# Performance work log

Hardware: AMD Instinct MI355X
Metric: run time of the kernel (lower is better)

## Reference

```python
import jax, jax.numpy as jnp
import numpy as np

EMBED = 64
HEADS = 4
HEAD_DIM = EMBED // HEADS
N, T = 1024, 36


def setup_inputs() -> dict:
    key = jax.random.key(0)
    ks = jax.random.split(key, 8)
    scale = 1.0 / np.sqrt(HEAD_DIM)
    return {
        "values": jax.random.normal(ks[0], (N, T, EMBED), dtype=jnp.float32),
        "keys": jax.random.normal(ks[1], (N, T, EMBED), dtype=jnp.float32),
        "query": jax.random.normal(ks[2], (N, T, EMBED), dtype=jnp.float32),
        "Wv": jax.random.normal(ks[3], (HEAD_DIM, HEAD_DIM), dtype=jnp.float32) * scale,
        "Wk": jax.random.normal(ks[4], (HEAD_DIM, HEAD_DIM), dtype=jnp.float32) * scale,
        "Wq": jax.random.normal(ks[5], (HEAD_DIM, HEAD_DIM), dtype=jnp.float32) * scale,
        "Wo": jax.random.normal(ks[6], (EMBED, EMBED), dtype=jnp.float32) * (1.0 / np.sqrt(EMBED)),
        "bo": jax.random.normal(ks[7], (EMBED,), dtype=jnp.float32) * 0.01,
    }


def reference(values, keys, query, Wv, Wk, Wq, Wo, bo):
    n, t, c = query.shape
    h, d = HEADS, HEAD_DIM
    v = values.reshape(n, t, h, d)
    k = keys.reshape(n, t, h, d)
    q = query.reshape(n, t, h, d)
    # nn.Linear(head_dim, head_dim, bias=False): x @ W.T
    v = jnp.einsum('nthd,ed->nthe', v, Wv)
    k = jnp.einsum('nthd,ed->nthe', k, Wk)
    q = jnp.einsum('nthd,ed->nthe', q, Wq)
    # attention over the node dim: energy [N_q, N_k, T, H]
    energy = jnp.einsum('qthd,kthd->qkth', q, k)
    attention = jax.nn.softmax(energy / jnp.sqrt(jnp.float32(c)), axis=1)
    out = jnp.einsum('qkth,kthd->qthd', attention, v).reshape(n, t, h * d)
    return out @ Wo.T + bo
```

## Files before the change

kernel.cpp:

```cpp
#include <hip/hip_runtime.h>
#include <math.h>

#define N_NODES 1024
#define T_STEPS 36
#define KTILE   128
#define KSTR2   24
#define VTSTR   136
#define WOS     72
#define OBS2    72

typedef __bf16  bf16x8 __attribute__((ext_vector_type(8)));
typedef float   f32x4  __attribute__((ext_vector_type(4)));

#define MFMA_BF16 __builtin_amdgcn_mfma_f32_16x16x32_bf16

__device__ __forceinline__ unsigned short bf16_rne(float f) {
    unsigned int u = __float_as_uint(f);
    u += 0x7FFFu + ((u >> 16) & 1u);
    return (unsigned short)(u >> 16);
}
__device__ __forceinline__ float bf16_tof(unsigned short h) {
    return __uint_as_float(((unsigned int)h) << 16);
}
__device__ __forceinline__ unsigned int bf16_bias(float f) {
    unsigned int u = __float_as_uint(f);
    return u + 0x7FFFu + ((u >> 16) & 1u);
}

__global__ __launch_bounds__(128) void proj4_kernel(
    const float* __restrict__ vin, const float* __restrict__ kin, const float* __restrict__ qin,
    const float* __restrict__ Wv, const float* __restrict__ Wk, const float* __restrict__ Wq,
    unsigned short* __restrict__ qhi, unsigned short* __restrict__ qlo,
    unsigned short* __restrict__ khi, unsigned short* __restrict__ klo,
    unsigned short* __restrict__ vthi, unsigned short* __restrict__ vtlo)
{
    __shared__ float sWv[256], sWk[256], sWq[256];
    const int tid = threadIdx.x;
    sWv[tid] = Wv[tid]; sWv[tid+128] = Wv[tid+128];
    sWk[tid] = Wk[tid]; sWk[tid+128] = Wk[tid+128];
    sWq[tid] = Wq[tid]; sWq[tid+128] = Wq[tid+128];
    __syncthreads();

    const int t = blockIdx.y;
    const int n = blockIdx.x * 128 + tid;
    const size_t ib = ((size_t)n * T_STEPS + t) * 64;
    const float QSCALE = 0.18033688011112042f;

    float x[64], y[4][16];

    #pragma unroll
    for (int i = 0; i < 16; ++i) { float4 f = *(const float4*)(qin + ib + 4*i);
        x[4*i]=f.x; x[4*i+1]=f.y; x[4*i+2]=f.z; x[4*i+3]=f.w; }
    #pragma unroll
    for (int e = 0; e < 16; ++e) {
        float4 w0 = *(const float4*)&sWq[e*16+0],  w1 = *(const float4*)&sWq[e*16+4];
        float4 w2 = *(const float4*)&sWq[e*16+8],  w3 = *(const float4*)&sWq[e*16+12];
        #pragma unroll
        for (int hd = 0; hd < 4; ++hd) {
            const float* xr = &x[hd*16];
            float a = xr[0]*w0.x;
            a = fmaf(xr[1],w0.y,a);  a = fmaf(xr[2],w0.z,a);  a = fmaf(xr[3],w0.w,a);
            a = fmaf(xr[4],w1.x,a);  a = fmaf(xr[5],w1.y,a);  a = fmaf(xr[6],w1.z,a);  a = fmaf(xr[7],w1.w,a);
            a = fmaf(xr[8],w2.x,a);  a = fmaf(xr[9],w2.y,a);  a = fmaf(xr[10],w2.z,a); a = fmaf(xr[11],w2.w,a);
            a = fmaf(xr[12],w3.x,a); a = fmaf(xr[13],w3.y,a); a = fmaf(xr[14],w3.z,a); a = fmaf(xr[15],w3.w,a);
            y[hd][e] = a * QSCALE;
        }
    }
    #pragma unroll
    for (int hd = 0; hd < 4; ++hd) {
        union { unsigned short u[16]; uint4 v[2]; } hb, lb;
        #pragma unroll
        for (int e = 0; e < 16; ++e) { unsigned short hh = bf16_rne(y[hd][e]);
            hb.u[e] = hh; lb.u[e] = bf16_rne(y[hd][e] - bf16_tof(hh)); }
        uint4* dh = (uint4*)(qhi + ((size_t)(t*4+hd)*N_NODES + n)*16);
        uint4* dl = (uint4*)(qlo + ((size_t)(t*4+hd)*N_NODES + n)*16);
        dh[0]=hb.v[0]; dh[1]=hb.v[1]; dl[0]=lb.v[0]; dl[1]=lb.v[1];
    }

    #pragma unroll
    for (int i = 0; i < 16; ++i) { float4 f = *(const float4*)(kin + ib + 4*i);
        x[4*i]=f.x; x[4*i+1]=f.y; x[4*i+2]=f.z; x[4*i+3]=f.w; }
    #pragma unroll
    for (int e = 0; e < 16; ++e) {
        float4 w0 = *(const float4*)&sWk[e*16+0],  w1 = *(const float4*)&sWk[e*16+4];
        float4 w2 = *(const float4*)&sWk[e*16+8],  w3 = *(const float4*)&sWk[e*16+12];
        #pragma unroll
        for (int hd = 0; hd < 4; ++hd) {
            const float* xr = &x[hd*16];
            float a = xr[0]*w0.x;
            a = fmaf(xr[1],w0.y,a);  a = fmaf(xr[2],w0.z,a);  a = fmaf(xr[3],w0.w,a);
            a = fmaf(xr[4],w1.x,a);  a = fmaf(xr[5],w1.y,a);  a = fmaf(xr[6],w1.z,a);  a = fmaf(xr[7],w1.w,a);
            a = fmaf(xr[8],w2.x,a);  a = fmaf(xr[9],w2.y,a);  a = fmaf(xr[10],w2.z,a); a = fmaf(xr[11],w2.w,a);
            a = fmaf(xr[12],w3.x,a); a = fmaf(xr[13],w3.y,a); a = fmaf(xr[14],w3.z,a); a = fmaf(xr[15],w3.w,a);
            y[hd][e] = a;
        }
    }
    #pragma unroll
    for (int hd = 0; hd < 4; ++hd) {
        union { unsigned short u[16]; uint4 v[2]; } hb, lb;
        #pragma unroll
        for (int e = 0; e < 16; ++e) { unsigned short hh = bf16_rne(y[hd][e]);
            hb.u[e] = hh; lb.u[e] = bf16_rne(y[hd][e] - bf16_tof(hh)); }
        uint4* dh = (uint4*)(khi + ((size_t)(t*4+hd)*N_NODES + n)*16);
        uint4* dl = (uint4*)(klo + ((size_t)(t*4+hd)*N_NODES + n)*16);
        dh[0]=hb.v[0]; dh[1]=hb.v[1]; dl[0]=lb.v[0]; dl[1]=lb.v[1];
    }

    #pragma unroll
    for (int i = 0; i < 16; ++i) { float4 f = *(const float4*)(vin + ib + 4*i);
        x[4*i]=f.x; x[4*i+1]=f.y; x[4*i+2]=f.z; x[4*i+3]=f.w; }
    #pragma unroll
    for (int e = 0; e < 16; ++e) {
        float4 w0 = *(const float4*)&sWv[e*16+0],  w1 = *(const float4*)&sWv[e*16+4];
        float4 w2 = *(const float4*)&sWv[e*16+8],  w3 = *(const float4*)&sWv[e*16+12];
        #pragma unroll
        for (int hd = 0; hd < 4; ++hd) {
            const float* xr = &x[hd*16];
            float a = xr[0]*w0.x;
            a = fmaf(xr[1],w0.y,a);  a = fmaf(xr[2],w0.z,a);  a = fmaf(xr[3],w0.w,a);
            a = fmaf(xr[4],w1.x,a);  a = fmaf(xr[5],w1.y,a);  a = fmaf(xr[6],w1.z,a);  a = fmaf(xr[7],w1.w,a);
            a = fmaf(xr[8],w2.x,a);  a = fmaf(xr[9],w2.y,a);  a = fmaf(xr[10],w2.z,a); a = fmaf(xr[11],w2.w,a);
            a = fmaf(xr[12],w3.x,a); a = fmaf(xr[13],w3.y,a); a = fmaf(xr[14],w3.z,a); a = fmaf(xr[15],w3.w,a);
            unsigned short hh = bf16_rne(a);
            const size_t off = ((size_t)(t*4+hd)*16 + e)*N_NODES + n;
            vthi[off] = hh;
            vtlo[off] = bf16_rne(a - bf16_tof(hh));
        }
    }
}

__global__ __launch_bounds__(256, 4) void attn_mfma3_kernel(
    const unsigned short* __restrict__ qhi, const unsigned short* __restrict__ qlo,
    const unsigned short* __restrict__ khi, const unsigned short* __restrict__ klo,
    const unsigned short* __restrict__ vthi, const unsigned short* __restrict__ vtlo,
    unsigned short* __restrict__ obh, unsigned short* __restrict__ obl)
{
    __shared__ unsigned short khi_s[KTILE * KSTR2];
    __shared__ unsigned short klo_s[KTILE * KSTR2];
    __shared__ unsigned short vthi_s[16 * VTSTR];
    __shared__ unsigned short vtlo_s[16 * VTSTR];

    const int tid  = threadIdx.x;
    const int wave = tid >> 6, lane = tid & 63;
    const int m = lane & 15, quad = lane >> 4;

    const int bid = blockIdx.x;
    const int th  = bid % 144;
    const int qb  = bid / 144;
    const int t   = th >> 2, hd = th & 3;
    const int q0  = qb * 128;
    const size_t base_th = (size_t)th * N_NODES;

    const bf16x8 bzero = {};
    bf16x8 b1q[2], b2q[2];
    #pragma unroll
    for (int g = 0; g < 2; ++g) {
        const int qrow = q0 + wave * 32 + g * 16 + m;
        b1q[g] = *(const bf16x8*)(qhi + (base_th + qrow) * 16 + (quad & 1) * 8);
        b2q[g] = (quad < 2)
            ? *(const bf16x8*)(qlo + (base_th + qrow) * 16 + (quad & 1) * 8) : bzero;
    }

    f32x4 og[2] = {{0.f,0.f,0.f,0.f},{0.f,0.f,0.f,0.f}};
    float lsum[2] = {0.f, 0.f};
    const unsigned short* kbase = (quad < 2) ? khi_s : klo_s;
    const int koff = m * KSTR2 + (quad & 1) * 8;
    const int voff = m * VTSTR + quad * 8;

    for (int kt = 0; kt < N_NODES; kt += KTILE) {
        __syncthreads();
        if (tid < 128) {
            const int r = tid;
            const uint4* gh = (const uint4*)(khi + (base_th + kt + r) * 16);
            const uint4* gl = (const uint4*)(klo + (base_th + kt + r) * 16);
            uint4 a0 = gh[0], a1 = gh[1], c0 = gl[0], c1 = gl[1];
            *(uint4*)&khi_s[r * KSTR2]     = a0;
            *(uint4*)&khi_s[r * KSTR2 + 8] = a1;
            *(uint4*)&klo_s[r * KSTR2]     = c0;
            *(uint4*)&klo_s[r * KSTR2 + 8] = c1;
        } else {
            const int j = tid - 128;
            const int sel = j >> 6, d = (j >> 2) & 15, part = j & 3;
            const unsigned short* src = (sel ? vtlo : vthi)
                + ((size_t)th * 16 + d) * N_NODES + kt + part * 32;
            unsigned short* dst = (sel ? vtlo_s : vthi_s) + d * VTSTR + part * 32;
            uint4 a0 = ((const uint4*)src)[0], a1 = ((const uint4*)src)[1];
            uint4 a2 = ((const uint4*)src)[2], a3 = ((const uint4*)src)[3];
            *(uint2*)&dst[0]  = make_uint2(a0.x, a0.y);
            *(uint2*)&dst[8]  = make_uint2(a0.z, a0.w);
            *(uint2*)&dst[16] = make_uint2(a1.x, a1.y);
            *(uint2*)&dst[24] = make_uint2(a1.z, a1.w);
            *(uint2*)&dst[4]  = make_uint2(a2.x, a2.y);
            *(uint2*)&dst[12] = make_uint2(a2.z, a2.w);
            *(uint2*)&dst[20] = make_uint2(a3.x, a3.y);
            *(uint2*)&dst[28] = make_uint2(a3.z, a3.w);
        }
        __syncthreads();

        #pragma unroll
        for (int c = 0; c < 4; ++c) {
            bf16x8 a0 = *(const bf16x8*)(kbase + (2*c    ) * 16 * KSTR2 + koff);
            bf16x8 a1 = *(const bf16x8*)(kbase + (2*c + 1) * 16 * KSTR2 + koff);
            unsigned int pk[2][4];
            #pragma unroll
            for (int g = 0; g < 2; ++g) {
                f32x4 s0 = MFMA_BF16(a0, b1q[g], (f32x4){0.f,0.f,0.f,0.f}, 0, 0, 0);
                s0 = MFMA_BF16(a0, b2q[g], s0, 0, 0, 0);
                f32x4 s1 = MFMA_BF16(a1, b1q[g], (f32x4){0.f,0.f,0.f,0.f}, 0, 0, 0);
                s1 = MFMA_BF16(a1, b2q[g], s1, 0, 0, 0);
                unsigned int u[8];
                float ls = 0.f;
                #pragma unroll
                for (int r = 0; r < 4; ++r) {
                    u[r]   = bf16_bias(__builtin_amdgcn_exp2f(s0[r]));
                    u[4+r] = bf16_bias(__builtin_amdgcn_exp2f(s1[r]));
                    ls += __uint_as_float(u[r]   & 0xFFFF0000u);
                    ls += __uint_as_float(u[4+r] & 0xFFFF0000u);
                }
                lsum[g] += ls;
                pk[g][0] = __builtin_amdgcn_perm(u[1], u[0], 0x07060302u);
                pk[g][1] = __builtin_amdgcn_perm(u[3], u[2], 0x07060302u);
                pk[g][2] = __builtin_amdgcn_perm(u[5], u[4], 0x07060302u);
                pk[g][3] = __builtin_amdgcn_perm(u[7], u[6], 0x07060302u);
            }
            bf16x8 vh = *(const bf16x8*)&vthi_s[voff + c * 32];
            bf16x8 vl = *(const bf16x8*)&vtlo_s[voff + c * 32];
            #pragma unroll
            for (int g = 0; g < 2; ++g) {
                union { unsigned int u[4]; bf16x8 v; } ap;
                ap.u[0] = pk[g][0]; ap.u[1] = pk[g][1];
                ap.u[2] = pk[g][2]; ap.u[3] = pk[g][3];
                og[g] = MFMA_BF16(ap.v, vh, og[g], 0, 0, 0);
                og[g] = MFMA_BF16(ap.v, vl, og[g], 0, 0, 0);
            }
        }
    }

    #pragma unroll
    for (int g = 0; g < 2; ++g) {
        lsum[g] += __shfl_xor(lsum[g], 16);
        lsum[g] += __shfl_xor(lsum[g], 32);
        #pragma unroll
        for (int r = 0; r < 4; ++r) {
            const float l = __shfl(lsum[g], quad * 4 + r);
            const float val = og[g][r] / l;
            const int row = q0 + wave * 32 + g * 16 + quad * 4 + r;
            const size_t off = ((size_t)row * T_STEPS + t) * 64 + hd * 16 + m;
            unsigned short hh = bf16_rne(val);
            obh[off] = hh;
            obl[off] = bf16_rne(val - bf16_tof(hh));
        }
    }
}

__global__ __launch_bounds__(256) void outproj_mfma_kernel(
    const unsigned short* __restrict__ obh, const unsigned short* __restrict__ obl,
    const float* __restrict__ Wo, const float* __restrict__ bo,
    float* __restrict__ out)
{
    __shared__ unsigned short woh[64 * WOS], wol[64 * WOS];
    __shared__ unsigned short oth[64 * OBS2], otl[64 * OBS2];
    __shared__ float sb[64];
    const int tid = threadIdx.x;

    #pragma unroll
    for (int i = 0; i < 16; ++i) {
        int idx = tid + 256 * i;
        int r = idx >> 6, c = idx & 63;
        float w = Wo[idx];
        unsigned short hh = bf16_rne(w);
        woh[r * WOS + c] = hh;
        wol[r * WOS + c] = bf16_rne(w - bf16_tof(hh));
    }
    if (tid < 64) sb[tid] = bo[tid];

    const size_t p0 = (size_t)blockIdx.x * 64;
    #pragma unroll
    for (int i = 0; i < 2; ++i) {
        int idx = tid + 256 * i;
        int r = idx >> 3, c = (idx & 7) * 8;
        *(uint4*)&oth[r * OBS2 + c] = *(const uint4*)(obh + (p0 + r) * 64 + c);
        *(uint4*)&otl[r * OBS2 + c] = *(const uint4*)(obl + (p0 + r) * 64 + c);
    }
    __syncthreads();

    const int wave = tid >> 6, lane = tid & 63;
    const int m = lane & 15, quad = lane >> 4;
    const int r0 = wave * 16;

    bf16x8 ah[2], al[2];
    #pragma unroll
    for (int kh = 0; kh < 2; ++kh) {
        ah[kh] = *(const bf16x8*)&oth[(r0 + m) * OBS2 + kh * 32 + quad * 8];
        al[kh] = *(const bf16x8*)&otl[(r0 + m) * OBS2 + kh * 32 + quad * 8];
    }

    f32x4 acc[4] = {{0,0,0,0},{0,0,0,0},{0,0,0,0},{0,0,0,0}};
    #pragma unroll
    for (int jt = 0; jt < 4; ++jt) {
        #pragma unroll
        for (int kh = 0; kh < 2; ++kh) {
            bf16x8 bh = *(const bf16x8*)&woh[(jt * 16 + m) * WOS + kh * 32 + quad * 8];
            bf16x8 bl = *(const bf16x8*)&wol[(jt * 16 + m) * WOS + kh * 32 + quad * 8];
            acc[jt] = MFMA_BF16(ah[kh], bh, acc[jt], 0, 0, 0);
            acc[jt] = MFMA_BF16(al[kh], bh, acc[jt], 0, 0, 0);
            acc[jt] = MFMA_BF16(ah[kh], bl, acc[jt], 0, 0, 0);
        }
    }

    #pragma unroll
    for (int jt = 0; jt < 4; ++jt) {
        const float b = sb[jt * 16 + m];
        #pragma unroll
        for (int r = 0; r < 4; ++r)
            out[(p0 + r0 + quad * 4 + r) * 64 + jt * 16 + m] = acc[jt][r] + b;
    }
}

extern "C" void kernel_launch(void* const* d_in, const int* in_sizes, int n_in,
                              void* d_out, int out_size, void* d_ws, size_t ws_size,
                              hipStream_t stream)
{
    (void)in_sizes; (void)n_in; (void)out_size; (void)ws_size;
    const float* values = (const float*)d_in[0];
    const float* keys   = (const float*)d_in[1];
    const float* query  = (const float*)d_in[2];
    const float* Wv     = (const float*)d_in[3];
    const float* Wk     = (const float*)d_in[4];
    const float* Wq     = (const float*)d_in[5];
    const float* Wo     = (const float*)d_in[6];
    const float* bo     = (const float*)d_in[7];

    const size_t TOT = (size_t)144 * N_NODES * 16;
    unsigned short* ws16 = (unsigned short*)d_ws;
    unsigned short* qhi  = ws16;
    unsigned short* qlo  = ws16 + 1*TOT;
    unsigned short* khi  = ws16 + 2*TOT;
    unsigned short* klo  = ws16 + 3*TOT;
    unsigned short* vthi = ws16 + 4*TOT;
    unsigned short* vtlo = ws16 + 5*TOT;
    unsigned short* obh  = ws16 + 6*TOT;
    unsigned short* obl  = ws16 + 7*TOT;

    proj4_kernel<<<dim3(8, 36), 128, 0, stream>>>(values, keys, query, Wv, Wk, Wq,
                                                  qhi, qlo, khi, klo, vthi, vtlo);
    attn_mfma3_kernel<<<dim3(8 * 144), 256, 0, stream>>>(qhi, qlo, khi, klo, vthi, vtlo,
                                                         obh, obl);
    outproj_mfma_kernel<<<dim3(576), 256, 0, stream>>>(obh, obl, Wo, bo, (float*)d_out);
}
```

Measured before the change: 156.3 us.

## Split projection per matrix and stage outputs in LDS for coalesced stores

The projection kernel now launches one block per (matrix, node tile, time pair) rather than one thread doing all three projections. Results are packed as hi/lo bf16 pairs into a padded shared-memory tile and then written out with 16-byte stores. For the transposed V layout this replaces scattered 2-byte global stores with coalesced vector stores. The grid also grows threefold for better occupancy, at the cost of extra shared memory and a block barrier.

```diff
diff --git a/kernel.cpp b/kernel.cpp
--- a/kernel.cpp
+++ b/kernel.cpp
@@ -8,11 +8,14 @@
 #define VTSTR   136
 #define WOS     72
 #define OBS2    72
+#define YSTR    67
 
 typedef __bf16  bf16x8 __attribute__((ext_vector_type(8)));
 typedef float   f32x4  __attribute__((ext_vector_type(4)));
 
 #define MFMA_BF16 __builtin_amdgcn_mfma_f32_16x16x32_bf16
+#define PERM_HI 0x07060302u
+#define PERM_LO 0x05040100u
 
 __device__ __forceinline__ unsigned short bf16_rne(float f) {
     unsigned int u = __float_as_uint(f);
@@ -26,105 +29,109 @@
     unsigned int u = __float_as_uint(f);
     return u + 0x7FFFu + ((u >> 16) & 1u);
 }
-
-__global__ __launch_bounds__(128) void proj4_kernel(
+__device__ __forceinline__ unsigned int split_pack(float a) {
+    unsigned short hi = bf16_rne(a);
+    unsigned short lo = bf16_rne(a - bf16_tof(hi));
+    return ((unsigned int)hi << 16) | lo;
+}
+
+__global__ __launch_bounds__(128) void proj5_kernel(
     const float* __restrict__ vin, const float* __restrict__ kin, const float* __restrict__ qin,
     const float* __restrict__ Wv, const float* __restrict__ Wk, const float* __restrict__ Wq,
     unsigned short* __restrict__ qhi, unsigned short* __restrict__ qlo,
     unsigned short* __restrict__ khi, unsigned short* __restrict__ klo,
     unsigned short* __restrict__ vthi, unsigned short* __restrict__ vtlo)
 {
-    __shared__ float sWv[256], sWk[256], sWq[256];
+    __shared__ float sW[256];
+    __shared__ unsigned int ys[128 * YSTR];
+
     const int tid = threadIdx.x;
-    sWv[tid] = Wv[tid]; sWv[tid+128] = Wv[tid+128];
-    sWk[tid] = Wk[tid]; sWk[tid+128] = Wk[tid+128];
-    sWq[tid] = Wq[tid]; sWq[tid+128] = Wq[tid+128];
+    const int mat = blockIdx.y;
+    const int nt  = blockIdx.x & 15;
+    const int tt  = blockIdx.x >> 4;
+    const int n0  = nt * 64, t0 = tt * 2;
+
+    const float* in = (mat == 0) ? vin : (mat == 1) ? kin : qin;
+    const float* W  = (mat == 0) ? Wv  : (mat == 1) ? Wk  : Wq;
+    sW[tid] = W[tid]; sW[tid + 128] = W[tid + 128];
     __syncthreads();
 
-    const int t = blockIdx.y;
-    const int n = blockIdx.x * 128 + tid;
-    const size_t ib = ((size_t)n * T_STEPS + t) * 64;
-    const float QSCALE = 0.18033688011112042f;
-
-    float x[64], y[4][16];
-
-    #pragma unroll
-    for (int i = 0; i < 16; ++i) { float4 f = *(const float4*)(qin + ib + 4*i);
-        x[4*i]=f.x; x[4*i+1]=f.y; x[4*i+2]=f.z; x[4*i+3]=f.w; }
-    #pragma unroll
-    for (int e = 0; e < 16; ++e) {
-        float4 w0 = *(const float4*)&sWq[e*16+0],  w1 = *(const float4*)&sWq[e*16+4];
-        float4 w2 = *(const float4*)&sWq[e*16+8],  w3 = *(const float4*)&sWq[e*16+12];
-        #pragma unroll
-        for (int hd = 0; hd < 4; ++hd) {
-            const float* xr = &x[hd*16];
-            float a = xr[0]*w0.x;
-            a = fmaf(xr[1],w0.y,a);  a = fmaf(xr[2],w0.z,a);  a = fmaf(xr[3],w0.w,a);
-            a = fmaf(xr[4],w1.x,a);  a = fmaf(xr[5],w1.y,a);  a = fmaf(xr[6],w1.z,a);  a = fmaf(xr[7],w1.w,a);
-            a = fmaf(xr[8],w2.x,a);  a = fmaf(xr[9],w2.y,a);  a = fmaf(xr[10],w2.z,a); a = fmaf(xr[11],w2.w,a);
-            a = fmaf(xr[12],w3.x,a); a = fmaf(xr[13],w3.y,a); a = fmaf(xr[14],w3.z,a); a = fmaf(xr[15],w3.w,a);
-            y[hd][e] = a * QSCALE;
-        }
-    }
-    #pragma unroll
-    for (int hd = 0; hd < 4; ++hd) {
-        union { unsigned short u[16]; uint4 v[2]; } hb, lb;
-        #pragma unroll
-        for (int e = 0; e < 16; ++e) { unsigned short hh = bf16_rne(y[hd][e]);
-            hb.u[e] = hh; lb.u[e] = bf16_rne(y[hd][e] - bf16_tof(hh)); }
-        uint4* dh = (uint4*)(qhi + ((size_t)(t*4+hd)*N_NODES + n)*16);
-        uint4* dl = (uint4*)(qlo + ((size_t)(t*4+hd)*N_NODES + n)*16);
-        dh[0]=hb.v[0]; dh[1]=hb.v[1]; dl[0]=lb.v[0]; dl[1]=lb.v[1];
-    }
-
-    #pragma unroll
-    for (int i = 0; i < 16; ++i) { float4 f = *(const float4*)(kin + ib + 4*i);
-        x[4*i]=f.x; x[4*i+1]=f.y; x[4*i+2]=f.z; x[4*i+3]=f.w; }
-    #pragma unroll
-    for (int e = 0; e < 16; ++e) {
-        float4 w0 = *(const float4*)&sWk[e*16+0],  w1 = *(const float4*)&sWk[e*16+4];
-        float4 w2 = *(const float4*)&sWk[e*16+8],  w3 = *(const float4*)&sWk[e*16+12];
-        #pragma unroll
-        for (int hd = 0; hd < 4; ++hd) {
-            const float* xr = &x[hd*16];
-            float a = xr[0]*w0.x;
-            a = fmaf(xr[1],w0.y,a);  a = fmaf(xr[2],w0.z,a);  a = fmaf(xr[3],w0.w,a);
-            a = fmaf(xr[4],w1.x,a);  a = fmaf(xr[5],w1.y,a);  a = fmaf(xr[6],w1.z,a);  a = fmaf(xr[7],w1.w,a);
-            a = fmaf(xr[8],w2.x,a);  a = fmaf(xr[9],w2.y,a);  a = fmaf(xr[10],w2.z,a); a = fmaf(xr[11],w2.w,a);
-            a = fmaf(xr[12],w3.x,a); a = fmaf(xr[13],w3.y,a); a = fmaf(xr[14],w3.z,a); a = fmaf(xr[15],w3.w,a);
-            y[hd][e] = a;
-        }
-    }
-    #pragma unroll
-    for (int hd = 0; hd < 4; ++hd) {
-        union { unsigned short u[16]; uint4 v[2]; } hb, lb;
-        #pragma unroll
-        for (int e = 0; e < 16; ++e) { unsigned short hh = bf16_rne(y[hd][e]);
-            hb.u[e] = hh; lb.u[e] = bf16_rne(y[hd][e] - bf16_tof(hh)); }
-        uint4* dh = (uint4*)(khi + ((size_t)(t*4+hd)*N_NODES + n)*16);
-        uint4* dl = (uint4*)(klo + ((size_t)(t*4+hd)*N_NODES + n)*16);
-        dh[0]=hb.v[0]; dh[1]=hb.v[1]; dl[0]=lb.v[0]; dl[1]=lb.v[1];
-    }
-
-    #pragma unroll
-    for (int i = 0; i < 16; ++i) { float4 f = *(const float4*)(vin + ib + 4*i);
-        x[4*i]=f.x; x[4*i+1]=f.y; x[4*i+2]=f.z; x[4*i+3]=f.w; }
-    #pragma unroll
-    for (int e = 0; e < 16; ++e) {
-        float4 w0 = *(const float4*)&sWv[e*16+0],  w1 = *(const float4*)&sWv[e*16+4];
-        float4 w2 = *(const float4*)&sWv[e*16+8],  w3 = *(const float4*)&sWv[e*16+12];
-        #pragma unroll
-        for (int hd = 0; hd < 4; ++hd) {
-            const float* xr = &x[hd*16];
-            float a = xr[0]*w0.x;
-            a = fmaf(xr[1],w0.y,a);  a = fmaf(xr[2],w0.z,a);  a = fmaf(xr[3],w0.w,a);
-            a = fmaf(xr[4],w1.x,a);  a = fmaf(xr[5],w1.y,a);  a = fmaf(xr[6],w1.z,a);  a = fmaf(xr[7],w1.w,a);
-            a = fmaf(xr[8],w2.x,a);  a = fmaf(xr[9],w2.y,a);  a = fmaf(xr[10],w2.z,a); a = fmaf(xr[11],w2.w,a);
-            a = fmaf(xr[12],w3.x,a); a = fmaf(xr[13],w3.y,a); a = fmaf(xr[14],w3.z,a); a = fmaf(xr[15],w3.w,a);
-            unsigned short hh = bf16_rne(a);
-            const size_t off = ((size_t)(t*4+hd)*16 + e)*N_NODES + n;
-            vthi[off] = hh;
-            vtlo[off] = bf16_rne(a - bf16_tof(hh));
+    {
+        const int nl = tid >> 1, tl = tid & 1;
+        const size_t p = ((size_t)(n0 + nl)) * T_STEPS + (t0 + tl);
+        const float4* src = (const float4*)(in + p * 64);
+        float x[64];
+        #pragma unroll
+        for (int i = 0; i < 16; ++i) {
+            float4 f = src[i];
+            x[4*i] = f.x; x[4*i+1] = f.y; x[4*i+2] = f.z; x[4*i+3] = f.w;
+        }
+        const float scale = (mat == 2) ? 0.18033688011112042f : 1.0f;
+        unsigned int* yrow = &ys[tid * YSTR];
+        #pragma unroll
+        for (int e = 0; e < 16; ++e) {
+            float4 w0 = *(const float4*)&sW[e*16+0],  w1 = *(const float4*)&sW[e*16+4];
+            float4 w2 = *(const float4*)&sW[e*16+8],  w3 = *(const float4*)&sW[e*16+12];
+            #pragma unroll
+            for (int hd = 0; hd < 4; ++hd) {
+                const float* xr = &x[hd*16];
+                float a = xr[0]*w0.x;
+                a = fmaf(xr[1],w0.y,a);  a = fmaf(xr[2],w0.z,a);  a = fmaf(xr[3],w0.w,a);
+                a = fmaf(xr[4],w1.x,a);  a = fmaf(xr[5],w1.y,a);  a = fmaf(xr[6],w1.z,a);  a = fmaf(xr[7],w1.w,a);
+                a = fmaf(xr[8],w2.x,a);  a = fmaf(xr[9],w2.y,a);  a = fmaf(xr[10],w2.z,a); a = fmaf(xr[11],w2.w,a);
+                a = fmaf(xr[12],w3.x,a); a = fmaf(xr[13],w3.y,a); a = fmaf(xr[14],w3.z,a); a = fmaf(xr[15],w3.w,a);
+                yrow[hd*16 + e] = split_pack(a * scale);
+            }
+        }
+    }
+    __syncthreads();
+
+    if (mat != 0) {
+        unsigned short* ohi = (mat == 1) ? khi : qhi;
+        unsigned short* olo = (mat == 1) ? klo : qlo;
+        const int nl2 = tid >> 1, eh = tid & 1;
+        #pragma unroll
+        for (int pass = 0; pass < 8; ++pass) {
+            const int tl2 = pass & 1, hd = pass >> 1;
+            const unsigned int* yr = &ys[(nl2*2 + tl2) * YSTR + hd*16 + eh*8];
+            unsigned int u0 = yr[0], u1 = yr[1], u2 = yr[2], u3 = yr[3];
+            unsigned int u4 = yr[4], u5 = yr[5], u6 = yr[6], u7 = yr[7];
+            uint4 hi4, lo4;
+            hi4.x = __builtin_amdgcn_perm(u1, u0, PERM_HI);
+            hi4.y = __builtin_amdgcn_perm(u3, u2, PERM_HI);
+            hi4.z = __builtin_amdgcn_perm(u5, u4, PERM_HI);
+            hi4.w = __builtin_amdgcn_perm(u7, u6, PERM_HI);
+            lo4.x = __builtin_amdgcn_perm(u1, u0, PERM_LO);
+            lo4.y = __builtin_amdgcn_perm(u3, u2, PERM_LO);
+            lo4.z = __builtin_amdgcn_perm(u5, u4, PERM_LO);
+            lo4.w = __builtin_amdgcn_perm(u7, u6, PERM_LO);
+            const int th = (t0 + tl2) * 4 + hd;
+            const size_t off = ((size_t)th * N_NODES + n0 + nl2) * 16 + eh * 8;
+            *(uint4*)(ohi + off) = hi4;
+            *(uint4*)(olo + off) = lo4;
+        }
+    } else {
+        const int e = tid >> 3, ng = tid & 7;
+        #pragma unroll
+        for (int pass = 0; pass < 8; ++pass) {
+            const int tl2 = pass & 1, hd = pass >> 1;
+            unsigned int u[8];
+            #pragma unroll
+            for (int j = 0; j < 8; ++j)
+                u[j] = ys[((ng*8 + j)*2 + tl2) * YSTR + hd*16 + e];
+            uint4 hi4, lo4;
+            hi4.x = __builtin_amdgcn_perm(u[1], u[0], PERM_HI);
+            hi4.y = __builtin_amdgcn_perm(u[3], u[2], PERM_HI);
+            hi4.z = __builtin_amdgcn_perm(u[5], u[4], PERM_HI);
+            hi4.w = __builtin_amdgcn_perm(u[7], u[6], PERM_HI);
+            lo4.x = __builtin_amdgcn_perm(u[1], u[0], PERM_LO);
+            lo4.y = __builtin_amdgcn_perm(u[3], u[2], PERM_LO);
+            lo4.z = __builtin_amdgcn_perm(u[5], u[4], PERM_LO);
+            lo4.w = __builtin_amdgcn_perm(u[7], u[6], PERM_LO);
+            const int th = (t0 + tl2) * 4 + hd;
+            const size_t off = ((size_t)th * 16 + e) * N_NODES + n0 + ng * 8;
+            *(uint4*)(vthi + off) = hi4;
+            *(uint4*)(vtlo + off) = lo4;
         }
     }
 }
@@ -218,10 +225,10 @@
                     ls += __uint_as_float(u[4+r] & 0xFFFF0000u);
                 }
                 lsum[g] += ls;
-                pk[g][0] = __builtin_amdgcn_perm(u[1], u[0], 0x07060302u);
-                pk[g][1] = __builtin_amdgcn_perm(u[3], u[2], 0x07060302u);
-                pk[g][2] = __builtin_amdgcn_perm(u[5], u[4], 0x07060302u);
-                pk[g][3] = __builtin_amdgcn_perm(u[7], u[6], 0x07060302u);
+                pk[g][0] = __builtin_amdgcn_perm(u[1], u[0], PERM_HI);
+                pk[g][1] = __builtin_amdgcn_perm(u[3], u[2], PERM_HI);
+                pk[g][2] = __builtin_amdgcn_perm(u[5], u[4], PERM_HI);
+                pk[g][3] = __builtin_amdgcn_perm(u[7], u[6], PERM_HI);
             }
             bf16x8 vh = *(const bf16x8*)&vthi_s[voff + c * 32];
             bf16x8 vl = *(const bf16x8*)&vtlo_s[voff + c * 32];
@@ -342,8 +349,8 @@
     unsigned short* obh  = ws16 + 6*TOT;
     unsigned short* obl  = ws16 + 7*TOT;
 
-    proj4_kernel<<<dim3(8, 36), 128, 0, stream>>>(values, keys, query, Wv, Wk, Wq,
-                                                  qhi, qlo, khi, klo, vthi, vtlo);
+    proj5_kernel<<<dim3(288, 3), 128, 0, stream>>>(values, keys, query, Wv, Wk, Wq,
+                                                   qhi, qlo, khi, klo, vthi, vtlo);
     attn_mfma3_kernel<<<dim3(8 * 144), 256, 0, stream>>>(qhi, qlo, khi, klo, vthi, vtlo,
                                                          obh, obl);
     outproj_mfma_kernel<<<dim3(576), 256, 0, stream>>>(obh, obl, Wo, bo, (float*)d_out);
```

Measured after the change: 145.9 us. 1.07x faster.
